# Performance work log

Hardware: AMD Instinct MI355X
Metric: run time of the kernel (lower is better)

## Reference

```python
import jax, jax.numpy as jnp
import numpy as np

IN_CH = 12
STEP = 4
UPLAG = 2048
HIDDEN = 1024
OUTPUT = 256
BATCH = 2048
FEAT = UPLAG // STEP  # per-channel conv output length


def setup_inputs() -> dict:
    key = jax.random.key(0)
    ks = jax.random.split(key, 7)
    s = 1.0 / np.sqrt(STEP)
    x = jax.random.normal(ks[0], (BATCH, IN_CH, UPLAG), dtype=jnp.float32)
    # per-channel Conv1d(1,1,step,step) weights/biases, stacked: [C, step], [C]
    W1 = jax.random.uniform(ks[1], (IN_CH, STEP), jnp.float32, -s, s)
    b1 = jax.random.uniform(ks[2], (IN_CH,), jnp.float32, -s, s)
    d_in = IN_CH * FEAT
    s2 = 1.0 / np.sqrt(d_in)
    W2 = jax.random.uniform(ks[3], (d_in, HIDDEN), jnp.float32, -s2, s2)
    b2 = jax.random.uniform(ks[4], (HIDDEN,), jnp.float32, -s2, s2)
    s3 = 1.0 / np.sqrt(HIDDEN)
    W3 = jax.random.uniform(ks[5], (HIDDEN, OUTPUT), jnp.float32, -s3, s3)
    b3 = jax.random.uniform(ks[6], (OUTPUT,), jnp.float32, -s3, s3)
    return {"x": x, "W1": W1, "b1": b1, "W2": W2, "b2": b2, "W3": W3, "b3": b3}


def reference(x, W1, b1, W2, b2, W3, b3):
    B, C, L = x.shape
    # Non-overlapping patch reduction equivalent to Conv1d(1,1,step,step) per channel:
    # view [B, C, F, step], contract step dim against per-channel kernel.
    xp = x.reshape(B, C, L // STEP, STEP)
    conv = jnp.einsum('bcfk,ck->bcf', xp, W1) + b1[None, :, None]  # [B, C, F]
    flat = conv.reshape(B, C * (L // STEP))  # concat order: channel-major, matches torch.cat
    h = jax.nn.relu(flat @ W2 + b2)
    out = h @ W3 + b3
    return out.reshape(B, 1, -1)
```

## Files before the change

kernel.cpp:

```cpp
#include <hip/hip_runtime.h>
#include <hip/hip_bf16.h>

#define BATCH   2048
#define IN_CH   12
#define UPLAG   2048
#define STEP    4
#define FEAT    512
#define DIN     6144
#define HIDDEN  1024
#define OUTPUT  256

typedef __bf16 bf16x8 __attribute__((ext_vector_type(8)));
typedef float  f32x4  __attribute__((ext_vector_type(4)));

__device__ __forceinline__ unsigned short f2bf(float f) {
  unsigned int u = __builtin_bit_cast(unsigned int, f);
  unsigned int r = (u + 0x7fffu + ((u >> 16) & 1u)) >> 16;
  return (unsigned short)r;
}

__device__ __forceinline__ float bf2f(unsigned short h) {
  unsigned int u = ((unsigned int)h) << 16;
  return __builtin_bit_cast(float, u);
}

__device__ __forceinline__ void async_copy16(const unsigned short* g, unsigned short* l) {
  __builtin_amdgcn_global_load_lds(
      (const __attribute__((address_space(1))) unsigned int*)g,
      (__attribute__((address_space(3))) unsigned int*)l, 16, 0, 0);
}

__global__ __launch_bounds__(256) void conv_cast_kernel(
    const float* __restrict__ x, const float* __restrict__ W1,
    const float* __restrict__ b1, unsigned short* __restrict__ out)
{
  int gid = blockIdx.x * 256 + threadIdx.x;
  const int total = BATCH * DIN;
  if (gid >= total) return;
  int cf = gid % DIN;
  int c  = cf >> 9;
  float4 xv = ((const float4*)x)[gid];
  float4 wv = ((const float4*)W1)[c];
  float v = xv.x * wv.x + xv.y * wv.y + xv.z * wv.z + xv.w * wv.w + b1[c];
  out[gid] = f2bf(v);
}

__global__ __launch_bounds__(256) void transpose_cast(
    const float* __restrict__ in, unsigned short* __restrict__ out,
    int R, int Ncol)
{
  __shared__ float tile[32][33];
  int bx = blockIdx.x * 32;
  int by = blockIdx.y * 32;
  int tx = threadIdx.x, ty = threadIdx.y;
  #pragma unroll
  for (int i = 0; i < 32; i += 8)
    tile[ty + i][tx] = in[(size_t)(by + ty + i) * Ncol + bx + tx];
  __syncthreads();
  #pragma unroll
  for (int i = 0; i < 32; i += 8)
    out[(size_t)(bx + ty + i) * R + by + tx] = f2bf(tile[tx][ty + i]);
}

#define G1_BM 128
#define G1_BN 128
#define G1_BK 32
#define SPLITK 6

__global__ __launch_bounds__(256, 2) void gemm1_kernel(
    const unsigned short* __restrict__ A,
    const unsigned short* __restrict__ BT,
    unsigned short* __restrict__ Cp,
    int M, int N, int K)
{
  __shared__ unsigned short As[G1_BM * G1_BK];
  __shared__ unsigned short Bs[G1_BN * G1_BK];
  const int t    = threadIdx.x;
  const int lane = t & 63;
  const int wave = t >> 6;

  int b    = blockIdx.x;
  int xcdg = b & 7;
  int rest = b >> 3;
  int xt   = rest & 7;
  int zz   = rest >> 3;
  int zt   = zz >> 1;
  int yt   = (xcdg << 1) | (zz & 1);

  const int m0 = yt * G1_BM;
  const int n0 = xt * G1_BN;
  const int Ks = K / SPLITK;
  const int kbeg = zt * Ks;

  const int wm = (wave >> 1) * 64;
  const int wn = (wave & 1) * 64;
  const int lm = lane & 15;
  const int lk = (lane >> 4) * 8;

  f32x4 acc[4][4];
  #pragma unroll
  for (int i = 0; i < 4; i++)
    #pragma unroll
    for (int j = 0; j < 4; j++) {
      f32x4 z = {0.f, 0.f, 0.f, 0.f};
      acc[i][j] = z;
    }

  const unsigned short* Ag = A  + (size_t)m0 * K + kbeg;
  const unsigned short* Bg = BT + (size_t)n0 * K + kbeg;

  for (int kk = 0; kk < Ks; kk += G1_BK) {
    #pragma unroll
    for (int r = 0; r < 2; ++r) {
      int chunk = r * 256 + t;
      int row = chunk >> 2;
      int kc  = (chunk & 3) * 8;
      async_copy16(Ag + (size_t)row * K + kk + kc, As + chunk * 8);
    }
    #pragma unroll
    for (int r = 0; r < 2; ++r) {
      int chunk = r * 256 + t;
      int row = chunk >> 2;
      int kc  = (chunk & 3) * 8;
      async_copy16(Bg + (size_t)row * K + kk + kc, Bs + chunk * 8);
    }
    __syncthreads();

    bf16x8 af[4], bfr[4];
    #pragma unroll
    for (int i = 0; i < 4; i++)
      af[i] = *(const bf16x8*)(As + (wm + i * 16 + lm) * G1_BK + lk);
    #pragma unroll
    for (int j = 0; j < 4; j++)
      bfr[j] = *(const bf16x8*)(Bs + (wn + j * 16 + lm) * G1_BK + lk);
    #pragma unroll
    for (int i = 0; i < 4; i++)
      #pragma unroll
      for (int j = 0; j < 4; j++)
        acc[i][j] = __builtin_amdgcn_mfma_f32_16x16x32_bf16(af[i], bfr[j], acc[i][j], 0, 0, 0);
    __syncthreads();
  }

  unsigned short* Co = Cp + (size_t)zt * M * N;
  const int rbase = (lane >> 4) * 4;
  #pragma unroll
  for (int i = 0; i < 4; i++)
    #pragma unroll
    for (int j = 0; j < 4; j++) {
      int col = n0 + wn + j * 16 + lm;
      #pragma unroll
      for (int r = 0; r < 4; r++) {
        int row = m0 + wm + i * 16 + rbase + r;
        Co[(size_t)row * N + col] = f2bf(acc[i][j][r]);
      }
    }
}

__global__ __launch_bounds__(256) void reduce_bias_relu(
    const unsigned short* __restrict__ Cp, const float* __restrict__ b2,
    unsigned short* __restrict__ H)
{
  const int MN = BATCH * HIDDEN;
  int i4 = blockIdx.x * 256 + threadIdx.x;
  if (i4 >= MN / 4) return;
  float4 s = {0.f, 0.f, 0.f, 0.f};
  #pragma unroll
  for (int p = 0; p < SPLITK; ++p) {
    ushort4 a = ((const ushort4*)(Cp + (size_t)p * MN))[i4];
    s.x += bf2f(a.x); s.y += bf2f(a.y); s.z += bf2f(a.z); s.w += bf2f(a.w);
  }
  int col = (i4 * 4) & (HIDDEN - 1);
  float4 bb = *(const float4*)(b2 + col);
  ushort4 o;
  o.x = f2bf(fmaxf(s.x + bb.x, 0.f));
  o.y = f2bf(fmaxf(s.y + bb.y, 0.f));
  o.z = f2bf(fmaxf(s.z + bb.z, 0.f));
  o.w = f2bf(fmaxf(s.w + bb.w, 0.f));
  ((ushort4*)H)[i4] = o;
}

#define SPLITK2 4

__global__ __launch_bounds__(256, 2) void gemm2_kernel(
    const unsigned short* __restrict__ A,
    const unsigned short* __restrict__ BT,
    unsigned short* __restrict__ Cp)
{
  const int M = BATCH, N = OUTPUT, K = HIDDEN;
  __shared__ unsigned short As[64 * 32];
  __shared__ unsigned short Bs[64 * 32];
  const int t    = threadIdx.x;
  const int lane = t & 63;
  const int wave = t >> 6;
  const int m0 = blockIdx.y * 64;
  const int n0 = blockIdx.x * 64;
  const int Ks = K / SPLITK2;
  const int kbeg = blockIdx.z * Ks;
  const int wm = (wave >> 1) * 32;
  const int wn = (wave & 1) * 32;
  const int lm = lane & 15;
  const int lk = (lane >> 4) * 8;
  const int row = t >> 2;
  const int kc  = (t & 3) * 8;

  f32x4 acc[2][2];
  #pragma unroll
  for (int i = 0; i < 2; i++)
    #pragma unroll
    for (int j = 0; j < 2; j++) {
      f32x4 z = {0.f, 0.f, 0.f, 0.f};
      acc[i][j] = z;
    }

  const unsigned short* Ag = A  + (size_t)m0 * K + kbeg;
  const unsigned short* Bg = BT + (size_t)n0 * K + kbeg;

  for (int kk = 0; kk < Ks; kk += 32) {
    async_copy16(Ag + (size_t)row * K + kk + kc, As + t * 8);
    async_copy16(Bg + (size_t)row * K + kk + kc, Bs + t * 8);
    __syncthreads();
    bf16x8 af[2], bfr[2];
    #pragma unroll
    for (int i = 0; i < 2; i++)
      af[i] = *(const bf16x8*)(As + (wm + i * 16 + lm) * 32 + lk);
    #pragma unroll
    for (int j = 0; j < 2; j++)
      bfr[j] = *(const bf16x8*)(Bs + (wn + j * 16 + lm) * 32 + lk);
    #pragma unroll
    for (int i = 0; i < 2; i++)
      #pragma unroll
      for (int j = 0; j < 2; j++)
        acc[i][j] = __builtin_amdgcn_mfma_f32_16x16x32_bf16(af[i], bfr[j], acc[i][j], 0, 0, 0);
    __syncthreads();
  }

  unsigned short* Co = Cp + (size_t)blockIdx.z * M * N;
  const int rbase = (lane >> 4) * 4;
  #pragma unroll
  for (int i = 0; i < 2; i++)
    #pragma unroll
    for (int j = 0; j < 2; j++) {
      int col = n0 + wn + j * 16 + lm;
      #pragma unroll
      for (int r = 0; r < 4; r++) {
        int row_o = m0 + wm + i * 16 + rbase + r;
        Co[(size_t)row_o * N + col] = f2bf(acc[i][j][r]);
      }
    }
}

__global__ __launch_bounds__(256) void reduce2_bias(
    const unsigned short* __restrict__ Cp, const float* __restrict__ b3,
    float* __restrict__ out)
{
  const int MN = BATCH * OUTPUT;
  int i4 = blockIdx.x * 256 + threadIdx.x;
  if (i4 >= MN / 4) return;
  float4 s = {0.f, 0.f, 0.f, 0.f};
  #pragma unroll
  for (int p = 0; p < SPLITK2; ++p) {
    ushort4 a = ((const ushort4*)(Cp + (size_t)p * MN))[i4];
    s.x += bf2f(a.x); s.y += bf2f(a.y); s.z += bf2f(a.z); s.w += bf2f(a.w);
  }
  int col = (i4 * 4) & (OUTPUT - 1);
  float4 bb = *(const float4*)(b3 + col);
  float4 o = {s.x + bb.x, s.y + bb.y, s.z + bb.z, s.w + bb.w};
  ((float4*)out)[i4] = o;
}

extern "C" void kernel_launch(void* const* d_in, const int* in_sizes, int n_in,
                              void* d_out, int out_size, void* d_ws, size_t ws_size,
                              hipStream_t stream)
{
  const float* x  = (const float*)d_in[0];
  const float* W1 = (const float*)d_in[1];
  const float* b1 = (const float*)d_in[2];
  const float* W2 = (const float*)d_in[3];
  const float* b2 = (const float*)d_in[4];
  const float* W3 = (const float*)d_in[5];
  const float* b3 = (const float*)d_in[6];
  float* out = (float*)d_out;

  char* ws = (char*)d_ws;
  unsigned short* flatA = (unsigned short*)ws; ws += (size_t)BATCH * DIN * 2;
  unsigned short* W2T   = (unsigned short*)ws; ws += (size_t)HIDDEN * DIN * 2;
  unsigned short* W3T   = (unsigned short*)ws; ws += (size_t)OUTPUT * HIDDEN * 2;
  unsigned short* Cpart = (unsigned short*)ws; ws += (size_t)SPLITK * BATCH * HIDDEN * 2;
  unsigned short* H     = (unsigned short*)ws; ws += (size_t)BATCH * HIDDEN * 2;
  unsigned short* Cp2   = (unsigned short*)ws; ws += (size_t)SPLITK2 * BATCH * OUTPUT * 2;

  conv_cast_kernel<<<(BATCH * DIN) / 256, 256, 0, stream>>>(x, W1, b1, flatA);
  transpose_cast<<<dim3(HIDDEN / 32, DIN / 32), dim3(32, 8), 0, stream>>>(W2, W2T, DIN, HIDDEN);
  transpose_cast<<<dim3(OUTPUT / 32, HIDDEN / 32), dim3(32, 8), 0, stream>>>(W3, W3T, HIDDEN, OUTPUT);
  gemm1_kernel<<<768, 256, 0, stream>>>(flatA, W2T, Cpart, BATCH, HIDDEN, DIN);
  reduce_bias_relu<<<(BATCH * HIDDEN / 4) / 256, 256, 0, stream>>>(Cpart, b2, H);
  gemm2_kernel<<<dim3(OUTPUT / 64, BATCH / 64, SPLITK2), 256, 0, stream>>>(H, W3T, Cp2);
  reduce2_bias<<<(BATCH * OUTPUT / 4) / 256, 256, 0, stream>>>(Cp2, b3, out);
}
```

Measured before the change: 351.4 us.

## Rewrite gemm1 as 256x256 tiles with double-buffered async-copy pipeline

```diff
diff --git a/kernel.cpp b/kernel.cpp
--- a/kernel.cpp
+++ b/kernel.cpp
@@ -62,96 +62,126 @@
     out[(size_t)(bx + ty + i) * R + by + tx] = f2bf(tile[tx][ty + i]);
 }
 
-#define G1_BM 128
-#define G1_BN 128
-#define G1_BK 32
-#define SPLITK 6
-
-__global__ __launch_bounds__(256, 2) void gemm1_kernel(
+#define SPLITK  8
+#define G1_KS   768
+#define G1_NTK  12
+
+__global__ __launch_bounds__(512, 2) void gemm1_kernel(
     const unsigned short* __restrict__ A,
     const unsigned short* __restrict__ BT,
     unsigned short* __restrict__ Cp,
     int M, int N, int K)
 {
-  __shared__ unsigned short As[G1_BM * G1_BK];
-  __shared__ unsigned short Bs[G1_BN * G1_BK];
+  __shared__ alignas(16) unsigned short As[2][2][256][32];
+  __shared__ alignas(16) unsigned short Bs[2][2][256][32];
+
   const int t    = threadIdx.x;
   const int lane = t & 63;
   const int wave = t >> 6;
-
-  int b    = blockIdx.x;
-  int xcdg = b & 7;
-  int rest = b >> 3;
-  int xt   = rest & 7;
-  int zz   = rest >> 3;
-  int zt   = zz >> 1;
-  int yt   = (xcdg << 1) | (zz & 1);
-
-  const int m0 = yt * G1_BM;
-  const int n0 = xt * G1_BN;
-  const int Ks = K / SPLITK;
-  const int kbeg = zt * Ks;
-
-  const int wm = (wave >> 1) * 64;
-  const int wn = (wave & 1) * 64;
-  const int lm = lane & 15;
-  const int lk = (lane >> 4) * 8;
-
-  f32x4 acc[4][4];
-  #pragma unroll
-  for (int i = 0; i < 4; i++)
+  const int wr   = wave >> 2;
+  const int wc   = wave & 3;
+  const int lm   = lane & 15;
+  const int hi2  = lane >> 4;
+
+  int bid  = blockIdx.x;
+  int xcd  = bid & 7;
+  int rest = bid >> 3;
+  int ml   = rest & 1;
+  int nl   = (rest >> 1) & 1;
+  int kz   = rest >> 2;
+  int yt   = (xcd >> 1) * 2 + ml;
+  int xt   = (xcd & 1) * 2 + nl;
+  const int m0   = yt * 256;
+  const int n0   = xt * 256;
+  const int kbeg = kz * G1_KS;
+
+  const unsigned short* Ag = A  + (size_t)m0 * K + kbeg;
+  const unsigned short* Bg = BT + (size_t)n0 * K + kbeg;
+
+  const int row0 = t >> 2;
+  const int cb0  = (t & 3) * 8;
+
+  auto stA = [&](int bf, int kh, int tt) {
+    unsigned short* l0 = &As[bf][kh][0][0];
+    const unsigned short* g = Ag + (size_t)tt * 64 + kh * 32;
+    async_copy16(g + (size_t)row0 * K + cb0,          l0 + t * 8);
+    async_copy16(g + (size_t)(row0 + 128) * K + cb0,  l0 + (t + 512) * 8);
+  };
+  auto stB = [&](int bf, int kh, int tt) {
+    unsigned short* l0 = &Bs[bf][kh][0][0];
+    const unsigned short* g = Bg + (size_t)tt * 64 + kh * 32;
+    async_copy16(g + (size_t)row0 * K + cb0,          l0 + t * 8);
+    async_copy16(g + (size_t)(row0 + 128) * K + cb0,  l0 + (t + 512) * 8);
+  };
+
+  f32x4 acc[8][4];
+  #pragma unroll
+  for (int i = 0; i < 8; i++)
     #pragma unroll
     for (int j = 0; j < 4; j++) {
       f32x4 z = {0.f, 0.f, 0.f, 0.f};
       acc[i][j] = z;
     }
 
-  const unsigned short* Ag = A  + (size_t)m0 * K + kbeg;
-  const unsigned short* Bg = BT + (size_t)n0 * K + kbeg;
-
-  for (int kk = 0; kk < Ks; kk += G1_BK) {
-    #pragma unroll
-    for (int r = 0; r < 2; ++r) {
-      int chunk = r * 256 + t;
-      int row = chunk >> 2;
-      int kc  = (chunk & 3) * 8;
-      async_copy16(Ag + (size_t)row * K + kk + kc, As + chunk * 8);
-    }
-    #pragma unroll
-    for (int r = 0; r < 2; ++r) {
-      int chunk = r * 256 + t;
-      int row = chunk >> 2;
-      int kc  = (chunk & 3) * 8;
-      async_copy16(Bg + (size_t)row * K + kk + kc, Bs + chunk * 8);
-    }
-    __syncthreads();
-
-    bf16x8 af[4], bfr[4];
-    #pragma unroll
-    for (int i = 0; i < 4; i++)
-      af[i] = *(const bf16x8*)(As + (wm + i * 16 + lm) * G1_BK + lk);
-    #pragma unroll
-    for (int j = 0; j < 4; j++)
-      bfr[j] = *(const bf16x8*)(Bs + (wn + j * 16 + lm) * G1_BK + lk);
-    #pragma unroll
-    for (int i = 0; i < 4; i++)
-      #pragma unroll
-      for (int j = 0; j < 4; j++)
-        acc[i][j] = __builtin_amdgcn_mfma_f32_16x16x32_bf16(af[i], bfr[j], acc[i][j], 0, 0, 0);
-    __syncthreads();
+  stA(0, 0, 0); stA(0, 1, 0); stB(0, 0, 0); stB(0, 1, 0);
+  stA(1, 0, 1); stB(1, 0, 1);
+  asm volatile("s_waitcnt vmcnt(4)" ::: "memory");
+  __builtin_amdgcn_sched_barrier(0);
+  __builtin_amdgcn_s_barrier();
+  __builtin_amdgcn_sched_barrier(0);
+
+  for (int tk = 0; tk < G1_NTK; ++tk) {
+    const int b   = tk & 1;
+    const int tn1 = (tk + 1 < G1_NTK) ? tk + 1 : G1_NTK - 1;
+    const int tn2 = (tk + 2 < G1_NTK) ? tk + 2 : G1_NTK - 1;
+    #pragma unroll
+    for (int p = 0; p < 4; ++p) {
+      const int kk = p >> 1;
+      const int mp = p & 1;
+
+      bf16x8 af[4], bfr[4];
+      #pragma unroll
+      for (int i = 0; i < 4; ++i)
+        af[i] = *(const bf16x8*)(&As[b][kk][wr * 128 + mp * 64 + i * 16 + lm][hi2 * 8]);
+      #pragma unroll
+      for (int j = 0; j < 4; ++j)
+        bfr[j] = *(const bf16x8*)(&Bs[b][kk][wc * 64 + j * 16 + lm][hi2 * 8]);
+
+      if      (p == 0) stA(1 - b, 1, tn1);
+      else if (p == 1) stB(1 - b, 1, tn1);
+      else if (p == 2) stA(b,     0, tn2);
+      else             stB(b,     0, tn2);
+
+      asm volatile("s_waitcnt vmcnt(6)" ::: "memory");
+      __builtin_amdgcn_sched_barrier(0);
+      __builtin_amdgcn_s_barrier();
+      __builtin_amdgcn_sched_barrier(0);
+
+      __builtin_amdgcn_s_setprio(1);
+      #pragma unroll
+      for (int i = 0; i < 4; ++i)
+        #pragma unroll
+        for (int j = 0; j < 4; ++j)
+          acc[mp * 4 + i][j] = __builtin_amdgcn_mfma_f32_16x16x32_bf16(
+              af[i], bfr[j], acc[mp * 4 + i][j], 0, 0, 0);
+      __builtin_amdgcn_s_setprio(0);
+      __builtin_amdgcn_sched_barrier(0);
+      __builtin_amdgcn_s_barrier();
+      __builtin_amdgcn_sched_barrier(0);
+    }
   }
 
-  unsigned short* Co = Cp + (size_t)zt * M * N;
+  unsigned short* Co = Cp + (size_t)kz * M * N;
   const int rbase = (lane >> 4) * 4;
   #pragma unroll
-  for (int i = 0; i < 4; i++)
-    #pragma unroll
-    for (int j = 0; j < 4; j++) {
-      int col = n0 + wn + j * 16 + lm;
-      #pragma unroll
-      for (int r = 0; r < 4; r++) {
-        int row = m0 + wm + i * 16 + rbase + r;
-        Co[(size_t)row * N + col] = f2bf(acc[i][j][r]);
+  for (int mi = 0; mi < 8; ++mi)
+    #pragma unroll
+    for (int j = 0; j < 4; ++j) {
+      int col = n0 + wc * 64 + j * 16 + lm;
+      #pragma unroll
+      for (int r = 0; r < 4; ++r) {
+        int row = m0 + wr * 128 + mi * 16 + rbase + r;
+        Co[(size_t)row * N + col] = f2bf(acc[mi][j][r]);
       }
     }
 }
@@ -292,7 +322,7 @@
   conv_cast_kernel<<<(BATCH * DIN) / 256, 256, 0, stream>>>(x, W1, b1, flatA);
   transpose_cast<<<dim3(HIDDEN / 32, DIN / 32), dim3(32, 8), 0, stream>>>(W2, W2T, DIN, HIDDEN);
   transpose_cast<<<dim3(OUTPUT / 32, HIDDEN / 32), dim3(32, 8), 0, stream>>>(W3, W3T, HIDDEN, OUTPUT);
-  gemm1_kernel<<<768, 256, 0, stream>>>(flatA, W2T, Cpart, BATCH, HIDDEN, DIN);
+  gemm1_kernel<<<256, 512, 0, stream>>>(flatA, W2T, Cpart, BATCH, HIDDEN, DIN);
   reduce_bias_relu<<<(BATCH * HIDDEN / 4) / 256, 256, 0, stream>>>(Cpart, b2, H);
   gemm2_kernel<<<dim3(OUTPUT / 64, BATCH / 64, SPLITK2), 256, 0, stream>>>(H, W3T, Cp2);
   reduce2_bias<<<(BATCH * OUTPUT / 4) / 256, 256, 0, stream>>>(Cp2, b3, out);
```

Measured after the change: 356.3 us. Within noise of the previous version (+1.4%).
